# Optimization experiments

Measured on AMD Instinct MI355X. Metric: run time of the kernel, lower is better.

Reference implementation:

```python
import jax, jax.numpy as jnp
import numpy as np

N = 100000      # nodes
E = 1600000     # edges (avg degree 16)
IN = 128        # in_channels
HID = 64        # hidden_channels
OUT = 96


def setup_inputs() -> dict:
    key = jax.random.key(0)
    k = jax.random.split(key, 5)
    x = jax.random.normal(k[0], (N, IN), dtype=jnp.float32)
    edge_index = jax.random.randint(k[1], (2, E), 0, N, dtype=jnp.int64)
    # GCNConv weights (glorot-ish scale) and biases
    W1 = jax.random.normal(k[2], (IN, HID), dtype=jnp.float32) / np.sqrt(IN).astype(np.float32)
    b1 = jnp.zeros((HID,), dtype=jnp.float32)
    W2 = jax.random.normal(k[3], (HID, OUT), dtype=jnp.float32) / np.sqrt(HID).astype(np.float32)
    b2 = jnp.zeros((OUT,), dtype=jnp.float32)
    return {"x": x, "edge_index": edge_index, "W1": W1, "b1": b1, "W2": W2, "b2": b2}


def _gcn_conv(x, W, b, src, dst, norm):
    # linear transform, then degree-normalized gather-scale-scatter aggregation
    h = x @ W                                   # [N, F]
    msg = h[src] * norm[:, None]                # [E+N, F]
    agg = jax.ops.segment_sum(msg, dst, num_segments=N)  # [N, F]
    return agg + b


def reference(x, edge_index, W1, b1, W2, b2):
    # add self-loops (PyG GCNConv default add_self_loops=True)
    loops = jnp.arange(N, dtype=edge_index.dtype)
    src = jnp.concatenate([edge_index[0], loops])
    dst = jnp.concatenate([edge_index[1], loops])
    # symmetric normalization: deg computed over destination (col) with unit weights
    deg = jax.ops.segment_sum(jnp.ones_like(dst, dtype=x.dtype), dst, num_segments=N)
    dinv = jnp.where(deg > 0, jax.lax.rsqrt(deg), 0.0)
    norm = dinv[src] * dinv[dst]                # [E+N]
    h = jax.nn.relu(_gcn_conv(x, W1, b1, src, dst, norm))
    # dropout is identity in eval mode
    out = _gcn_conv(h, W2, b2, src, dst, norm)  # [N, OUT]
    return out
```

## Files before the change

### kernel.cpp

```cpp
#include <hip/hip_runtime.h>
#include <hip/hip_fp16.h>


#define IN_F  128
#define HID_F 64
#define OUT_F 96
#define CHUNK 4096
#define MAXB  12288
#define AGG_BLOCKS 4096
#define ONE_LO 0x00003C00u
#define ONE_HI 0x3C000000u

typedef _Float16 f16x2 __attribute__((ext_vector_type(2)));
typedef _Float16 half8 __attribute__((ext_vector_type(8)));
typedef float floatx4 __attribute__((ext_vector_type(4)));

__device__ __forceinline__ float2 unpack2(unsigned u) {
    __half2 h = *reinterpret_cast<__half2*>(&u);
    return __half22float2(h);
}
__device__ __forceinline__ unsigned f2h2(float lo, float hi) {
    __half2 h = __floats2half2_rn(lo, hi);
    return *reinterpret_cast<unsigned*>(&h);
}

#if defined(__has_builtin)
#if __has_builtin(__builtin_amdgcn_fdot2)
#define HAS_FDOT2 1
#endif
#if __has_builtin(__builtin_amdgcn_mfma_f32_16x16x32_f16)
#define HAS_MFMA 1
#endif
#endif
#ifndef HAS_FDOT2
#define HAS_FDOT2 0
#endif
#ifndef HAS_MFMA
#define HAS_MFMA 0
#endif

__device__ __forceinline__ float fdot2u(unsigned a, unsigned b, float c) {
#if HAS_FDOT2
    return __builtin_amdgcn_fdot2(__builtin_bit_cast(f16x2, a),
                                  __builtin_bit_cast(f16x2, b), c, false);
#else
    float2 fa = unpack2(a), fb = unpack2(b);
    return fmaf(fa.y, fb.y, fmaf(fa.x, fb.x, c));
#endif
}

__global__ __launch_bounds__(64) void init_sentinel(unsigned* __restrict__ hs,
                                                    unsigned* __restrict__ hs2, int n) {
    int t = threadIdx.x;
    if (t < 32) {
        hs[(size_t)n * 32 + t] = 0u;
        hs2[(size_t)n * 32 + t] = 0u;
    }
}

__global__ __launch_bounds__(256) void hist_chunks(const int* __restrict__ dst,
                                                   int* __restrict__ hist,
                                                   int E, int nbuck, int nchunk) {
    __shared__ int cnt[512];
    for (int i = threadIdx.x; i < nbuck; i += 256) cnt[i] = 0;
    __syncthreads();
    const int base = blockIdx.x * CHUNK;
    const int lim = min(base + CHUNK, E);
    for (int e = base + threadIdx.x; e < lim; e += 256)
        atomicAdd(&cnt[dst[e] >> 8], 1);
    __syncthreads();
    for (int b = threadIdx.x; b < nbuck; b += 256)
        hist[b * nchunk + blockIdx.x] = cnt[b];
}

__global__ __launch_bounds__(256) void scan_blocks(const int* __restrict__ in,
                                                   int* __restrict__ pre,
                                                   int* __restrict__ bsum, int m) {
    __shared__ int lds[256];
    const int t = threadIdx.x;
    const int base = blockIdx.x * 1024 + t * 4;
    int v0 = (base + 0 < m) ? in[base + 0] : 0;
    int v1 = (base + 1 < m) ? in[base + 1] : 0;
    int v2 = (base + 2 < m) ? in[base + 2] : 0;
    int v3 = (base + 3 < m) ? in[base + 3] : 0;
    int s = v0 + v1 + v2 + v3;
    lds[t] = s;
    __syncthreads();
    for (int off = 1; off < 256; off <<= 1) {
        int add = (t >= off) ? lds[t - off] : 0;
        __syncthreads();
        lds[t] += add;
        __syncthreads();
    }
    int e = lds[t] - s;
    if (base + 0 < m) pre[base + 0] = e;
    e += v0;
    if (base + 1 < m) pre[base + 1] = e;
    e += v1;
    if (base + 2 < m) pre[base + 2] = e;
    e += v2;
    if (base + 3 < m) pre[base + 3] = e;
    if (t == 255) bsum[blockIdx.x] = lds[255];
}

__global__ __launch_bounds__(256) void scan_bsums(const int* __restrict__ bsum,
                                                  int* __restrict__ boffs, int nb) {
    __shared__ int lds[256];
    const int t = threadIdx.x;
    int v = (t < nb) ? bsum[t] : 0;
    lds[t] = v;
    __syncthreads();
    for (int off = 1; off < 256; off <<= 1) {
        int add = (t >= off) ? lds[t - off] : 0;
        __syncthreads();
        lds[t] += add;
        __syncthreads();
    }
    boffs[t] = lds[t] - v;
}

__global__ __launch_bounds__(256) void partition(const int* __restrict__ src,
                                                 const int* __restrict__ dst,
                                                 const int* __restrict__ offs,
                                                 const int* __restrict__ boffs,
                                                 unsigned* __restrict__ part,
                                                 int E, int nbuck, int nchunk) {
    __shared__ int off[512];
    for (int b = threadIdx.x; b < nbuck; b += 256) {
        int idx = b * nchunk + blockIdx.x;
        off[b] = offs[idx] + boffs[idx >> 10];
    }
    __syncthreads();
    const int base = blockIdx.x * CHUNK;
    const int lim = min(base + CHUNK, E);
    for (int e = base + threadIdx.x; e < lim; e += 256) {
        int d = dst[e], s = src[e];
        int pos = atomicAdd(&off[d >> 8], 1);
        part[pos] = ((unsigned)s << 8) | (unsigned)(d & 255);
    }
}

__global__ __launch_bounds__(256) void build_bucket(const unsigned* __restrict__ part,
                                                    const int* __restrict__ offs,
                                                    const int* __restrict__ boffs,
                                                    int* __restrict__ csr_src,
                                                    int4* __restrict__ nodetab,
                                                    float* __restrict__ dinv,
                                                    int n, int E, int nbuck, int nchunk) {
    __shared__ int cnt[256], sc[256], off[256];
    __shared__ int stage[MAXB];
    const int b = blockIdx.x;
    const int t = threadIdx.x;
    const int i0 = b * nchunk;
    const int bstart = offs[i0] + boffs[i0 >> 10];
    int bend = E;
    if (b + 1 < nbuck) {
        const int i1 = (b + 1) * nchunk;
        bend = offs[i1] + boffs[i1 >> 10];
    }
    const int bstart_pad = bstart + b * 4096;
    const int nodebase = b << 8;
    const int nnodes = min(256, n - nodebase);

    cnt[t] = 0;
    __syncthreads();
    for (int i = bstart + t; i < bend; i += 256)
        atomicAdd(&cnt[part[i] & 255u], 1);
    __syncthreads();
    const int deg = cnt[t];
    const int pdeg = (deg + 15) & ~15;
    sc[t] = pdeg;
    __syncthreads();
    for (int o = 1; o < 256; o <<= 1) {
        int add = (t >= o) ? sc[t - o] : 0;
        __syncthreads();
        sc[t] += add;
        __syncthreads();
    }
    const int pexcl = sc[t] - pdeg;
    const int psize = sc[255];
    if (t < nnodes) {
        float dv = rsqrtf((float)(deg + 1));
        nodetab[nodebase + t] = make_int4(bstart_pad + pexcl,
                                          bstart_pad + pexcl + pdeg,
                                          __float_as_int(dv), 0);
        dinv[nodebase + t] = dv;
    }
    off[t] = pexcl;
    __syncthreads();

    if (psize <= MAXB) {
        for (int i = t; i < psize; i += 256) stage[i] = n;
        __syncthreads();
        for (int i = bstart + t; i < bend; i += 256) {
            unsigned r = part[i];
            int pos = atomicAdd(&off[r & 255u], 1);
            stage[pos] = (int)(r >> 8);
        }
        __syncthreads();
        for (int i = t; i < psize; i += 256)
            csr_src[bstart_pad + i] = stage[i];
    } else {
        for (int i = t; i < psize; i += 256) csr_src[bstart_pad + i] = n;
        __syncthreads();
        for (int i = bstart + t; i < bend; i += 256) {
            unsigned r = part[i];
            int pos = atomicAdd(&off[r & 255u], 1);
            csr_src[bstart_pad + pos] = (int)(r >> 8);
        }
    }
}

__global__ __launch_bounds__(256) void gemm1(const float* __restrict__ x,
                                             const float* __restrict__ W1,
                                             const float* __restrict__ dinv,
                                             unsigned* __restrict__ hs, int n) {
#if HAS_MFMA
    const int lane = threadIdx.x & 63;
    const int wave = threadIdx.x >> 6;
    const int q4 = lane >> 4;
    const int l16 = lane & 15;
    half8 bfrag[4][4];
#pragma unroll
    for (int ks = 0; ks < 4; ++ks)
#pragma unroll
        for (int cb = 0; cb < 4; ++cb)
#pragma unroll
            for (int j = 0; j < 8; ++j)
                bfrag[ks][cb][j] =
                    (_Float16)W1[(ks * 32 + q4 * 8 + j) * HID_F + cb * 16 + l16];

    const int ntile = (n + 15) >> 4;
    for (int t = blockIdx.x * 4 + wave; t < ntile; t += gridDim.x * 4) {
        const int r0 = t << 4;
        const int arow = min(r0 + l16, n - 1);
        const float* xr = x + (size_t)arow * IN_F + q4 * 8;
        half8 afrag[4];
#pragma unroll
        for (int ks = 0; ks < 4; ++ks) {
            float4 v0 = *(const float4*)(xr + ks * 32);
            float4 v1 = *(const float4*)(xr + ks * 32 + 4);
            half8 a;
            a[0] = (_Float16)v0.x; a[1] = (_Float16)v0.y;
            a[2] = (_Float16)v0.z; a[3] = (_Float16)v0.w;
            a[4] = (_Float16)v1.x; a[5] = (_Float16)v1.y;
            a[6] = (_Float16)v1.z; a[7] = (_Float16)v1.w;
            afrag[ks] = a;
        }
        floatx4 acc[4] = {{0.f,0.f,0.f,0.f},{0.f,0.f,0.f,0.f},
                          {0.f,0.f,0.f,0.f},{0.f,0.f,0.f,0.f}};
#pragma unroll
        for (int ks = 0; ks < 4; ++ks) {
#pragma unroll
            for (int cb = 0; cb < 4; ++cb)
                acc[cb] = __builtin_amdgcn_mfma_f32_16x16x32_f16(
                    afrag[ks], bfrag[ks][cb], acc[cb], 0, 0, 0);
        }
        const int rbase = r0 + q4 * 4;
        float4 dvv = *(const float4*)(dinv + rbase);
        float dvr[4] = {dvv.x, dvv.y, dvv.z, dvv.w};
#pragma unroll
        for (int cb = 0; cb < 4; ++cb) {
#pragma unroll
            for (int reg = 0; reg < 4; ++reg) {
                float v = acc[cb][reg] * dvr[reg];
                float o = __shfl_xor(v, 1);
                if (!(l16 & 1)) {
                    int r = rbase + reg;
                    if (r < n)
                        hs[(size_t)r * 32 + cb * 8 + (l16 >> 1)] = f2h2(v, o);
                }
            }
        }
    }
#endif
}

#define ACC2(u, slo, shi) { slo = fdot2u(u, ONE_LO, slo); shi = fdot2u(u, ONE_HI, shi); }
template <int LAYER>
__global__ __launch_bounds__(256) void csr_agg(const int4* __restrict__ nodetab,
                                               const int* __restrict__ csr_src,
                                               const unsigned* __restrict__ hs,
                                               const float* __restrict__ bias,
                                               unsigned* __restrict__ hout, int n) {
    const int lane = threadIdx.x & 63;
    const int g = lane >> 4;
    const int w = lane & 15;
    const unsigned* __restrict__ hw = hs + 2 * w;
    const int STR = gridDim.x * 16;
    const int SENT = n;

    for (int base = (blockIdx.x * 4 + (threadIdx.x >> 6)) * 4; base < n; base += STR) {
        int pp0, pp1, pp2, pp3, ee0, ee1, ee2, ee3;
        float dn0, dn1, dn2, dn3;
        {
            int4 nt0 = nodetab[base];
            pp0 = nt0.x; ee0 = nt0.y; dn0 = __int_as_float(nt0.z);
        }
        if (base + 1 < n) { int4 v = nodetab[base + 1]; pp1 = v.x; ee1 = v.y; dn1 = __int_as_float(v.z); }
        else { pp1 = 0; ee1 = 0; dn1 = 0.f; }
        if (base + 2 < n) { int4 v = nodetab[base + 2]; pp2 = v.x; ee2 = v.y; dn2 = __int_as_float(v.z); }
        else { pp2 = 0; ee2 = 0; dn2 = 0.f; }
        if (base + 3 < n) { int4 v = nodetab[base + 3]; pp3 = v.x; ee3 = v.y; dn3 = __int_as_float(v.z); }
        else { pp3 = 0; ee3 = 0; dn3 = 0.f; }

        float a00 = 0.f, a01 = 0.f, a02 = 0.f, a03 = 0.f;
        float a10 = 0.f, a11 = 0.f, a12 = 0.f, a13 = 0.f;
        float a20 = 0.f, a21 = 0.f, a22 = 0.f, a23 = 0.f;
        float a30 = 0.f, a31 = 0.f, a32 = 0.f, a33 = 0.f;
        if (g == 0) {
            int s0 = base;
            int s1 = (base + 1 < n) ? base + 1 : SENT;
            int s2 = (base + 2 < n) ? base + 2 : SENT;
            int s3 = (base + 3 < n) ? base + 3 : SENT;
            uint2 u0 = *(const uint2*)(hw + (size_t)s0 * 32);
            uint2 u1 = *(const uint2*)(hw + (size_t)s1 * 32);
            uint2 u2 = *(const uint2*)(hw + (size_t)s2 * 32);
            uint2 u3 = *(const uint2*)(hw + (size_t)s3 * 32);
            ACC2(u0.x, a00, a01); ACC2(u0.y, a02, a03);
            ACC2(u1.x, a10, a11); ACC2(u1.y, a12, a13);
            ACC2(u2.x, a20, a21); ACC2(u2.y, a22, a23);
            ACC2(u3.x, a30, a31); ACC2(u3.y, a32, a33);
        }
        while ((pp0 < ee0) | (pp1 < ee1) | (pp2 < ee2) | (pp3 < ee3)) {
            int4 iv0 = (pp0 < ee0) ? *(const int4*)&csr_src[pp0 + 4 * g]
                                   : make_int4(SENT, SENT, SENT, SENT);
            int4 iv1 = (pp1 < ee1) ? *(const int4*)&csr_src[pp1 + 4 * g]
                                   : make_int4(SENT, SENT, SENT, SENT);
            int4 iv2 = (pp2 < ee2) ? *(const int4*)&csr_src[pp2 + 4 * g]
                                   : make_int4(SENT, SENT, SENT, SENT);
            int4 iv3 = (pp3 < ee3) ? *(const int4*)&csr_src[pp3 + 4 * g]
                                   : make_int4(SENT, SENT, SENT, SENT);
            uint2 u00 = *(const uint2*)(hw + (size_t)iv0.x * 32);
            uint2 u01 = *(const uint2*)(hw + (size_t)iv0.y * 32);
            uint2 u02 = *(const uint2*)(hw + (size_t)iv0.z * 32);
            uint2 u03 = *(const uint2*)(hw + (size_t)iv0.w * 32);
            uint2 u10 = *(const uint2*)(hw + (size_t)iv1.x * 32);
            uint2 u11 = *(const uint2*)(hw + (size_t)iv1.y * 32);
            uint2 u12 = *(const uint2*)(hw + (size_t)iv1.z * 32);
            uint2 u13 = *(const uint2*)(hw + (size_t)iv1.w * 32);
            uint2 u20 = *(const uint2*)(hw + (size_t)iv2.x * 32);
            uint2 u21 = *(const uint2*)(hw + (size_t)iv2.y * 32);
            uint2 u22 = *(const uint2*)(hw + (size_t)iv2.z * 32);
            uint2 u23 = *(const uint2*)(hw + (size_t)iv2.w * 32);
            uint2 u30 = *(const uint2*)(hw + (size_t)iv3.x * 32);
            uint2 u31 = *(const uint2*)(hw + (size_t)iv3.y * 32);
            uint2 u32 = *(const uint2*)(hw + (size_t)iv3.z * 32);
            uint2 u33 = *(const uint2*)(hw + (size_t)iv3.w * 32);
            ACC2(u00.x, a00, a01); ACC2(u00.y, a02, a03);
            ACC2(u01.x, a00, a01); ACC2(u01.y, a02, a03);
            ACC2(u02.x, a00, a01); ACC2(u02.y, a02, a03);
            ACC2(u03.x, a00, a01); ACC2(u03.y, a02, a03);
            ACC2(u10.x, a10, a11); ACC2(u10.y, a12, a13);
            ACC2(u11.x, a10, a11); ACC2(u11.y, a12, a13);
            ACC2(u12.x, a10, a11); ACC2(u12.y, a12, a13);
            ACC2(u13.x, a10, a11); ACC2(u13.y, a12, a13);
            ACC2(u20.x, a20, a21); ACC2(u20.y, a22, a23);
            ACC2(u21.x, a20, a21); ACC2(u21.y, a22, a23);
            ACC2(u22.x, a20, a21); ACC2(u22.y, a22, a23);
            ACC2(u23.x, a20, a21); ACC2(u23.y, a22, a23);
            ACC2(u30.x, a30, a31); ACC2(u30.y, a32, a33);
            ACC2(u31.x, a30, a31); ACC2(u31.y, a32, a33);
            ACC2(u32.x, a30, a31); ACC2(u32.y, a32, a33);
            ACC2(u33.x, a30, a31); ACC2(u33.y, a32, a33);
            pp0 += 16; pp1 += 16; pp2 += 16; pp3 += 16;
        }
        a00 += __shfl_xor(a00, 16); a00 += __shfl_xor(a00, 32);
        a01 += __shfl_xor(a01, 16); a01 += __shfl_xor(a01, 32);
        a02 += __shfl_xor(a02, 16); a02 += __shfl_xor(a02, 32);
        a03 += __shfl_xor(a03, 16); a03 += __shfl_xor(a03, 32);
        a10 += __shfl_xor(a10, 16); a10 += __shfl_xor(a10, 32);
        a11 += __shfl_xor(a11, 16); a11 += __shfl_xor(a11, 32);
        a12 += __shfl_xor(a12, 16); a12 += __shfl_xor(a12, 32);
        a13 += __shfl_xor(a13, 16); a13 += __shfl_xor(a13, 32);
        a20 += __shfl_xor(a20, 16); a20 += __shfl_xor(a20, 32);
        a21 += __shfl_xor(a21, 16); a21 += __shfl_xor(a21, 32);
        a22 += __shfl_xor(a22, 16); a22 += __shfl_xor(a22, 32);
        a23 += __shfl_xor(a23, 16); a23 += __shfl_xor(a23, 32);
        a30 += __shfl_xor(a30, 16); a30 += __shfl_xor(a30, 32);
        a31 += __shfl_xor(a31, 16); a31 += __shfl_xor(a31, 32);
        a32 += __shfl_xor(a32, 16); a32 += __shfl_xor(a32, 32);
        a33 += __shfl_xor(a33, 16); a33 += __shfl_xor(a33, 32);

        if (g == 0) {
            float4 bb;
            if (LAYER == 1) bb = *(const float4*)(bias + 4 * w);
#define EPI(i, dn, v0, v1, v2, v3)                                          \
            if (base + i < n) {                                             \
                float o0, o1, o2, o3;                                       \
                if (LAYER == 1) {                                           \
                    o0 = fmaxf(fmaf(dn, v0, bb.x), 0.f) * dn;               \
                    o1 = fmaxf(fmaf(dn, v1, bb.y), 0.f) * dn;               \
                    o2 = fmaxf(fmaf(dn, v2, bb.z), 0.f) * dn;               \
                    o3 = fmaxf(fmaf(dn, v3, bb.w), 0.f) * dn;               \
                } else {                                                    \
                    o0 = dn * v0; o1 = dn * v1; o2 = dn * v2; o3 = dn * v3; \
                }                                                           \
                uint2 ov;                                                   \
                ov.x = f2h2(o0, o1);                                        \
                ov.y = f2h2(o2, o3);                                        \
                *(uint2*)(hout + (size_t)(base + i) * 32 + 2 * w) = ov;     \
            }
            EPI(0, dn0, a00, a01, a02, a03)
            EPI(1, dn1, a10, a11, a12, a13)
            EPI(2, dn2, a20, a21, a22, a23)
            EPI(3, dn3, a30, a31, a32, a33)
#undef EPI
        }
    }
}

__global__ __launch_bounds__(256) void gemm2(const unsigned* __restrict__ a2h,
                                             const float* __restrict__ W2,
                                             const float* __restrict__ b2,
                                             float* __restrict__ out, int n) {
#if HAS_MFMA
    const int lane = threadIdx.x & 63;
    const int wave = threadIdx.x >> 6;
    const int q4 = lane >> 4;
    const int l16 = lane & 15;
    half8 bfrag[2][6];
#pragma unroll
    for (int ks = 0; ks < 2; ++ks)
#pragma unroll
        for (int cb = 0; cb < 6; ++cb)
#pragma unroll
            for (int j = 0; j < 8; ++j)
                bfrag[ks][cb][j] =
                    (_Float16)W2[(ks * 32 + q4 * 8 + j) * OUT_F + cb * 16 + l16];
    float bb[6];
#pragma unroll
    for (int cb = 0; cb < 6; ++cb) bb[cb] = b2[cb * 16 + l16];

    const int ntile = (n + 15) >> 4;
    for (int t = blockIdx.x * 4 + wave; t < ntile; t += gridDim.x * 4) {
        const int r0 = t << 4;
        const int arow = min(r0 + l16, n - 1);
        const unsigned* ar = a2h + (size_t)arow * 32;
        half8 afrag[2];
#pragma unroll
        for (int ks = 0; ks < 2; ++ks) {
            uint4 v = *(const uint4*)(ar + ks * 16 + q4 * 4);
            afrag[ks] = __builtin_bit_cast(half8, v);
        }
        floatx4 acc[6] = {{0.f,0.f,0.f,0.f},{0.f,0.f,0.f,0.f},{0.f,0.f,0.f,0.f},
                          {0.f,0.f,0.f,0.f},{0.f,0.f,0.f,0.f},{0.f,0.f,0.f,0.f}};
#pragma unroll
        for (int ks = 0; ks < 2; ++ks) {
#pragma unroll
            for (int cb = 0; cb < 6; ++cb)
                acc[cb] = __builtin_amdgcn_mfma_f32_16x16x32_f16(
                    afrag[ks], bfrag[ks][cb], acc[cb], 0, 0, 0);
        }
        const int rbase = r0 + q4 * 4;
#pragma unroll
        for (int reg = 0; reg < 4; ++reg) {
            int r = rbase + reg;
            if (r < n) {
#pragma unroll
                for (int cb = 0; cb < 6; ++cb)
                    out[(size_t)r * OUT_F + cb * 16 + l16] = acc[cb][reg] + bb[cb];
            }
        }
    }
#endif
}

extern "C" void kernel_launch(void* const* d_in, const int* in_sizes, int n_in,
                              void* d_out, int out_size, void* d_ws, size_t ws_size,
                              hipStream_t stream) {
    const float* x  = (const float*)d_in[0];
    const int*   ei = (const int*)d_in[1];
    const float* W1 = (const float*)d_in[2];
    const float* b1 = (const float*)d_in[3];
    const float* W2 = (const float*)d_in[4];
    const float* b2 = (const float*)d_in[5];
    float* out = (float*)d_out;

    const int n = in_sizes[0] / IN_F;
    const int E = in_sizes[1] / 2;
    const int* src = ei;
    const int* dst = ei + E;
    const int nbuck  = (n + 255) >> 8;
    const int nchunk = (E + CHUNK - 1) / CHUNK;
    const int M = nbuck * nchunk;
    const int NBS = (M + 1023) / 1024;
    const int g1tiles = (n + 15) / 16;
    const int g1blocks = (g1tiles + 7) / 8;

    char* ws = (char*)d_ws;
    size_t off = 0;
    auto alloc = [&](size_t bytes) { void* p = ws + off; off = (off + bytes + 255) & ~(size_t)255; return p; };
    int*      hist    = (int*)alloc((size_t)M * 4);
    int*      offs    = (int*)alloc((size_t)M * 4);
    int*      bsum    = (int*)alloc(256 * 4);
    int*      boffs   = (int*)alloc(256 * 4);
    unsigned* part    = (unsigned*)alloc((size_t)E * 4);
    int*      csr_src = (int*)alloc(((size_t)E + (size_t)nbuck * 4096 + 64) * 4);
    int4*     nodetab = (int4*)alloc((size_t)n * 16);
    float*    dinv    = (float*)alloc((size_t)n * 4);
    unsigned* hs      = (unsigned*)alloc((size_t)(n + 1) * 32 * 4);
    unsigned* hs2     = (unsigned*)alloc((size_t)(n + 1) * 32 * 4);
    unsigned* a2h     = (unsigned*)alloc((size_t)n * 32 * 4);

    init_sentinel<<<1, 64, 0, stream>>>(hs, hs2, n);
    hist_chunks <<<nchunk, 256, 0, stream>>>(dst, hist, E, nbuck, nchunk);
    scan_blocks <<<NBS, 256, 0, stream>>>(hist, offs, bsum, M);
    scan_bsums  <<<1, 256, 0, stream>>>(bsum, boffs, NBS);
    partition   <<<nchunk, 256, 0, stream>>>(src, dst, offs, boffs, part, E, nbuck, nchunk);
    build_bucket<<<nbuck, 256, 0, stream>>>(part, offs, boffs, csr_src, nodetab, dinv,
                                            n, E, nbuck, nchunk);

    gemm1      <<<g1blocks, 256, 0, stream>>>(x, W1, dinv, hs, n);
    csr_agg<1> <<<AGG_BLOCKS, 256, 0, stream>>>(nodetab, csr_src, hs, b1, hs2, n);
    csr_agg<2> <<<AGG_BLOCKS, 256, 0, stream>>>(nodetab, csr_src, hs2, NULL, a2h, n);
    gemm2      <<<g1blocks, 256, 0, stream>>>(a2h, W2, b2, out, n);
}
```

Before: 158.9 us.

## Restructure CSR aggregation to 2 nodes per wave with 16-byte row gathers

The aggregation kernel now gives each wave 2 nodes instead of 4. Each row is split over 8 lanes that each load a uint4 (16 B) instead of 16 lanes loading uint2, so each lane group consumes 2 edges per step and 8 groups cover 16 edges. It also prefetches the next node-table entries before processing the current pair, to hide that latency. The aim is wider gather loads, fewer wasted sentinel loads on imbalanced degrees, and overlapped index fetching. In exchange the shuffle reduction gains a stage, there is less memory-level parallelism per wave, and a grid-stride loop with software prefetch is added.

```diff
diff --git a/kernel.cpp b/kernel.cpp
--- a/kernel.cpp
+++ b/kernel.cpp
@@ -284,129 +284,134 @@
                                                const float* __restrict__ bias,
                                                unsigned* __restrict__ hout, int n) {
     const int lane = threadIdx.x & 63;
-    const int g = lane >> 4;
-    const int w = lane & 15;
-    const unsigned* __restrict__ hw = hs + 2 * w;
-    const int STR = gridDim.x * 16;
+    const int g = lane >> 3;
+    const int w = lane & 7;
+    const uint4* __restrict__ hw4 = (const uint4*)hs + w;
+    const int STR = gridDim.x * 8;
     const int SENT = n;
 
-    for (int base = (blockIdx.x * 4 + (threadIdx.x >> 6)) * 4; base < n; base += STR) {
-        int pp0, pp1, pp2, pp3, ee0, ee1, ee2, ee3;
-        float dn0, dn1, dn2, dn3;
-        {
-            int4 nt0 = nodetab[base];
-            pp0 = nt0.x; ee0 = nt0.y; dn0 = __int_as_float(nt0.z);
-        }
-        if (base + 1 < n) { int4 v = nodetab[base + 1]; pp1 = v.x; ee1 = v.y; dn1 = __int_as_float(v.z); }
-        else { pp1 = 0; ee1 = 0; dn1 = 0.f; }
-        if (base + 2 < n) { int4 v = nodetab[base + 2]; pp2 = v.x; ee2 = v.y; dn2 = __int_as_float(v.z); }
-        else { pp2 = 0; ee2 = 0; dn2 = 0.f; }
-        if (base + 3 < n) { int4 v = nodetab[base + 3]; pp3 = v.x; ee3 = v.y; dn3 = __int_as_float(v.z); }
-        else { pp3 = 0; ee3 = 0; dn3 = 0.f; }
-
-        float a00 = 0.f, a01 = 0.f, a02 = 0.f, a03 = 0.f;
-        float a10 = 0.f, a11 = 0.f, a12 = 0.f, a13 = 0.f;
-        float a20 = 0.f, a21 = 0.f, a22 = 0.f, a23 = 0.f;
-        float a30 = 0.f, a31 = 0.f, a32 = 0.f, a33 = 0.f;
+    int nodeA = (blockIdx.x * 4 + (threadIdx.x >> 6)) * 2;
+    if (nodeA >= n) return;
+    int4 ntA = nodetab[nodeA];
+    bool hasB = nodeA + 1 < n;
+    int4 ntB = hasB ? nodetab[nodeA + 1] : make_int4(0, 0, 0, 0);
+
+    for (;;) {
+        const int nxt = nodeA + STR;
+        const bool more = nxt < n;
+        int4 ntA_n, ntB_n;
+        bool hasB_n = false;
+        if (more) {
+            ntA_n = nodetab[nxt];
+            hasB_n = nxt + 1 < n;
+            if (hasB_n) ntB_n = nodetab[nxt + 1];
+        }
+
+        int pA = ntA.x;
+        const int endA = ntA.y;
+        const float dnA = __int_as_float(ntA.z);
+        int pB = hasB ? ntB.x : 0;
+        const int endB = hasB ? ntB.y : 0;
+        const float dnB = hasB ? __int_as_float(ntB.z) : 0.f;
+
+        float aA0 = 0.f, aA1 = 0.f, aA2 = 0.f, aA3 = 0.f;
+        float aA4 = 0.f, aA5 = 0.f, aA6 = 0.f, aA7 = 0.f;
+        float aB0 = 0.f, aB1 = 0.f, aB2 = 0.f, aB3 = 0.f;
+        float aB4 = 0.f, aB5 = 0.f, aB6 = 0.f, aB7 = 0.f;
         if (g == 0) {
-            int s0 = base;
-            int s1 = (base + 1 < n) ? base + 1 : SENT;
-            int s2 = (base + 2 < n) ? base + 2 : SENT;
-            int s3 = (base + 3 < n) ? base + 3 : SENT;
-            uint2 u0 = *(const uint2*)(hw + (size_t)s0 * 32);
-            uint2 u1 = *(const uint2*)(hw + (size_t)s1 * 32);
-            uint2 u2 = *(const uint2*)(hw + (size_t)s2 * 32);
-            uint2 u3 = *(const uint2*)(hw + (size_t)s3 * 32);
-            ACC2(u0.x, a00, a01); ACC2(u0.y, a02, a03);
-            ACC2(u1.x, a10, a11); ACC2(u1.y, a12, a13);
-            ACC2(u2.x, a20, a21); ACC2(u2.y, a22, a23);
-            ACC2(u3.x, a30, a31); ACC2(u3.y, a32, a33);
-        }
-        while ((pp0 < ee0) | (pp1 < ee1) | (pp2 < ee2) | (pp3 < ee3)) {
-            int4 iv0 = (pp0 < ee0) ? *(const int4*)&csr_src[pp0 + 4 * g]
-                                   : make_int4(SENT, SENT, SENT, SENT);
-            int4 iv1 = (pp1 < ee1) ? *(const int4*)&csr_src[pp1 + 4 * g]
-                                   : make_int4(SENT, SENT, SENT, SENT);
-            int4 iv2 = (pp2 < ee2) ? *(const int4*)&csr_src[pp2 + 4 * g]
-                                   : make_int4(SENT, SENT, SENT, SENT);
-            int4 iv3 = (pp3 < ee3) ? *(const int4*)&csr_src[pp3 + 4 * g]
-                                   : make_int4(SENT, SENT, SENT, SENT);
-            uint2 u00 = *(const uint2*)(hw + (size_t)iv0.x * 32);
-            uint2 u01 = *(const uint2*)(hw + (size_t)iv0.y * 32);
-            uint2 u02 = *(const uint2*)(hw + (size_t)iv0.z * 32);
-            uint2 u03 = *(const uint2*)(hw + (size_t)iv0.w * 32);
-            uint2 u10 = *(const uint2*)(hw + (size_t)iv1.x * 32);
-            uint2 u11 = *(const uint2*)(hw + (size_t)iv1.y * 32);
-            uint2 u12 = *(const uint2*)(hw + (size_t)iv1.z * 32);
-            uint2 u13 = *(const uint2*)(hw + (size_t)iv1.w * 32);
-            uint2 u20 = *(const uint2*)(hw + (size_t)iv2.x * 32);
-            uint2 u21 = *(const uint2*)(hw + (size_t)iv2.y * 32);
-            uint2 u22 = *(const uint2*)(hw + (size_t)iv2.z * 32);
-            uint2 u23 = *(const uint2*)(hw + (size_t)iv2.w * 32);
-            uint2 u30 = *(const uint2*)(hw + (size_t)iv3.x * 32);
-            uint2 u31 = *(const uint2*)(hw + (size_t)iv3.y * 32);
-            uint2 u32 = *(const uint2*)(hw + (size_t)iv3.z * 32);
-            uint2 u33 = *(const uint2*)(hw + (size_t)iv3.w * 32);
-            ACC2(u00.x, a00, a01); ACC2(u00.y, a02, a03);
-            ACC2(u01.x, a00, a01); ACC2(u01.y, a02, a03);
-            ACC2(u02.x, a00, a01); ACC2(u02.y, a02, a03);
-            ACC2(u03.x, a00, a01); ACC2(u03.y, a02, a03);
-            ACC2(u10.x, a10, a11); ACC2(u10.y, a12, a13);
-            ACC2(u11.x, a10, a11); ACC2(u11.y, a12, a13);
-            ACC2(u12.x, a10, a11); ACC2(u12.y, a12, a13);
-            ACC2(u13.x, a10, a11); ACC2(u13.y, a12, a13);
-            ACC2(u20.x, a20, a21); ACC2(u20.y, a22, a23);
-            ACC2(u21.x, a20, a21); ACC2(u21.y, a22, a23);
-            ACC2(u22.x, a20, a21); ACC2(u22.y, a22, a23);
-            ACC2(u23.x, a20, a21); ACC2(u23.y, a22, a23);
-            ACC2(u30.x, a30, a31); ACC2(u30.y, a32, a33);
-            ACC2(u31.x, a30, a31); ACC2(u31.y, a32, a33);
-            ACC2(u32.x, a30, a31); ACC2(u32.y, a32, a33);
-            ACC2(u33.x, a30, a31); ACC2(u33.y, a32, a33);
-            pp0 += 16; pp1 += 16; pp2 += 16; pp3 += 16;
-        }
-        a00 += __shfl_xor(a00, 16); a00 += __shfl_xor(a00, 32);
-        a01 += __shfl_xor(a01, 16); a01 += __shfl_xor(a01, 32);
-        a02 += __shfl_xor(a02, 16); a02 += __shfl_xor(a02, 32);
-        a03 += __shfl_xor(a03, 16); a03 += __shfl_xor(a03, 32);
-        a10 += __shfl_xor(a10, 16); a10 += __shfl_xor(a10, 32);
-        a11 += __shfl_xor(a11, 16); a11 += __shfl_xor(a11, 32);
-        a12 += __shfl_xor(a12, 16); a12 += __shfl_xor(a12, 32);
-        a13 += __shfl_xor(a13, 16); a13 += __shfl_xor(a13, 32);
-        a20 += __shfl_xor(a20, 16); a20 += __shfl_xor(a20, 32);
-        a21 += __shfl_xor(a21, 16); a21 += __shfl_xor(a21, 32);
-        a22 += __shfl_xor(a22, 16); a22 += __shfl_xor(a22, 32);
-        a23 += __shfl_xor(a23, 16); a23 += __shfl_xor(a23, 32);
-        a30 += __shfl_xor(a30, 16); a30 += __shfl_xor(a30, 32);
-        a31 += __shfl_xor(a31, 16); a31 += __shfl_xor(a31, 32);
-        a32 += __shfl_xor(a32, 16); a32 += __shfl_xor(a32, 32);
-        a33 += __shfl_xor(a33, 16); a33 += __shfl_xor(a33, 32);
+            uint4 suA = hw4[(size_t)nodeA * 8];
+            ACC2(suA.x, aA0, aA1); ACC2(suA.y, aA2, aA3);
+            ACC2(suA.z, aA4, aA5); ACC2(suA.w, aA6, aA7);
+            if (hasB) {
+                uint4 suB = hw4[(size_t)(nodeA + 1) * 8];
+                ACC2(suB.x, aB0, aB1); ACC2(suB.y, aB2, aB3);
+                ACC2(suB.z, aB4, aB5); ACC2(suB.w, aB6, aB7);
+            }
+        }
+        while (pA < endA || pB < endB) {
+            int2 ivA = (pA < endA) ? *(const int2*)&csr_src[pA + 2 * g]
+                                   : make_int2(SENT, SENT);
+            int2 ivB = (pB < endB) ? *(const int2*)&csr_src[pB + 2 * g]
+                                   : make_int2(SENT, SENT);
+            uint4 uA0 = hw4[(size_t)ivA.x * 8];
+            uint4 uA1 = hw4[(size_t)ivA.y * 8];
+            uint4 uB0 = hw4[(size_t)ivB.x * 8];
+            uint4 uB1 = hw4[(size_t)ivB.y * 8];
+            ACC2(uA0.x, aA0, aA1); ACC2(uA0.y, aA2, aA3);
+            ACC2(uA0.z, aA4, aA5); ACC2(uA0.w, aA6, aA7);
+            ACC2(uA1.x, aA0, aA1); ACC2(uA1.y, aA2, aA3);
+            ACC2(uA1.z, aA4, aA5); ACC2(uA1.w, aA6, aA7);
+            ACC2(uB0.x, aB0, aB1); ACC2(uB0.y, aB2, aB3);
+            ACC2(uB0.z, aB4, aB5); ACC2(uB0.w, aB6, aB7);
+            ACC2(uB1.x, aB0, aB1); ACC2(uB1.y, aB2, aB3);
+            ACC2(uB1.z, aB4, aB5); ACC2(uB1.w, aB6, aB7);
+            pA += 16; pB += 16;
+        }
+        aA0 += __shfl_xor(aA0, 8); aA0 += __shfl_xor(aA0, 16); aA0 += __shfl_xor(aA0, 32);
+        aA1 += __shfl_xor(aA1, 8); aA1 += __shfl_xor(aA1, 16); aA1 += __shfl_xor(aA1, 32);
+        aA2 += __shfl_xor(aA2, 8); aA2 += __shfl_xor(aA2, 16); aA2 += __shfl_xor(aA2, 32);
+        aA3 += __shfl_xor(aA3, 8); aA3 += __shfl_xor(aA3, 16); aA3 += __shfl_xor(aA3, 32);
+        aA4 += __shfl_xor(aA4, 8); aA4 += __shfl_xor(aA4, 16); aA4 += __shfl_xor(aA4, 32);
+        aA5 += __shfl_xor(aA5, 8); aA5 += __shfl_xor(aA5, 16); aA5 += __shfl_xor(aA5, 32);
+        aA6 += __shfl_xor(aA6, 8); aA6 += __shfl_xor(aA6, 16); aA6 += __shfl_xor(aA6, 32);
+        aA7 += __shfl_xor(aA7, 8); aA7 += __shfl_xor(aA7, 16); aA7 += __shfl_xor(aA7, 32);
+        aB0 += __shfl_xor(aB0, 8); aB0 += __shfl_xor(aB0, 16); aB0 += __shfl_xor(aB0, 32);
+        aB1 += __shfl_xor(aB1, 8); aB1 += __shfl_xor(aB1, 16); aB1 += __shfl_xor(aB1, 32);
+        aB2 += __shfl_xor(aB2, 8); aB2 += __shfl_xor(aB2, 16); aB2 += __shfl_xor(aB2, 32);
+        aB3 += __shfl_xor(aB3, 8); aB3 += __shfl_xor(aB3, 16); aB3 += __shfl_xor(aB3, 32);
+        aB4 += __shfl_xor(aB4, 8); aB4 += __shfl_xor(aB4, 16); aB4 += __shfl_xor(aB4, 32);
+        aB5 += __shfl_xor(aB5, 8); aB5 += __shfl_xor(aB5, 16); aB5 += __shfl_xor(aB5, 32);
+        aB6 += __shfl_xor(aB6, 8); aB6 += __shfl_xor(aB6, 16); aB6 += __shfl_xor(aB6, 32);
+        aB7 += __shfl_xor(aB7, 8); aB7 += __shfl_xor(aB7, 16); aB7 += __shfl_xor(aB7, 32);
 
         if (g == 0) {
-            float4 bb;
-            if (LAYER == 1) bb = *(const float4*)(bias + 4 * w);
-#define EPI(i, dn, v0, v1, v2, v3)                                          \
-            if (base + i < n) {                                             \
-                float o0, o1, o2, o3;                                       \
-                if (LAYER == 1) {                                           \
-                    o0 = fmaxf(fmaf(dn, v0, bb.x), 0.f) * dn;               \
-                    o1 = fmaxf(fmaf(dn, v1, bb.y), 0.f) * dn;               \
-                    o2 = fmaxf(fmaf(dn, v2, bb.z), 0.f) * dn;               \
-                    o3 = fmaxf(fmaf(dn, v3, bb.w), 0.f) * dn;               \
-                } else {                                                    \
-                    o0 = dn * v0; o1 = dn * v1; o2 = dn * v2; o3 = dn * v3; \
-                }                                                           \
-                uint2 ov;                                                   \
-                ov.x = f2h2(o0, o1);                                        \
-                ov.y = f2h2(o2, o3);                                        \
-                *(uint2*)(hout + (size_t)(base + i) * 32 + 2 * w) = ov;     \
+            float4 bb0, bb1;
+            if (LAYER == 1) {
+                bb0 = *(const float4*)(bias + 8 * w);
+                bb1 = *(const float4*)(bias + 8 * w + 4);
             }
-            EPI(0, dn0, a00, a01, a02, a03)
-            EPI(1, dn1, a10, a11, a12, a13)
-            EPI(2, dn2, a20, a21, a22, a23)
-            EPI(3, dn3, a30, a31, a32, a33)
-#undef EPI
-        }
+            float o0, o1, o2, o3, o4, o5, o6, o7;
+            if (LAYER == 1) {
+                o0 = fmaxf(fmaf(dnA, aA0, bb0.x), 0.f) * dnA;
+                o1 = fmaxf(fmaf(dnA, aA1, bb0.y), 0.f) * dnA;
+                o2 = fmaxf(fmaf(dnA, aA2, bb0.z), 0.f) * dnA;
+                o3 = fmaxf(fmaf(dnA, aA3, bb0.w), 0.f) * dnA;
+                o4 = fmaxf(fmaf(dnA, aA4, bb1.x), 0.f) * dnA;
+                o5 = fmaxf(fmaf(dnA, aA5, bb1.y), 0.f) * dnA;
+                o6 = fmaxf(fmaf(dnA, aA6, bb1.z), 0.f) * dnA;
+                o7 = fmaxf(fmaf(dnA, aA7, bb1.w), 0.f) * dnA;
+            } else {
+                o0 = dnA * aA0; o1 = dnA * aA1; o2 = dnA * aA2; o3 = dnA * aA3;
+                o4 = dnA * aA4; o5 = dnA * aA5; o6 = dnA * aA6; o7 = dnA * aA7;
+            }
+            uint4 ov;
+            ov.x = f2h2(o0, o1); ov.y = f2h2(o2, o3);
+            ov.z = f2h2(o4, o5); ov.w = f2h2(o6, o7);
+            *(uint4*)(hout + (size_t)nodeA * 32 + 4 * w) = ov;
+            if (hasB) {
+                if (LAYER == 1) {
+                    o0 = fmaxf(fmaf(dnB, aB0, bb0.x), 0.f) * dnB;
+                    o1 = fmaxf(fmaf(dnB, aB1, bb0.y), 0.f) * dnB;
+                    o2 = fmaxf(fmaf(dnB, aB2, bb0.z), 0.f) * dnB;
+                    o3 = fmaxf(fmaf(dnB, aB3, bb0.w), 0.f) * dnB;
+                    o4 = fmaxf(fmaf(dnB, aB4, bb1.x), 0.f) * dnB;
+                    o5 = fmaxf(fmaf(dnB, aB5, bb1.y), 0.f) * dnB;
+                    o6 = fmaxf(fmaf(dnB, aB6, bb1.z), 0.f) * dnB;
+                    o7 = fmaxf(fmaf(dnB, aB7, bb1.w), 0.f) * dnB;
+                } else {
+                    o0 = dnB * aB0; o1 = dnB * aB1; o2 = dnB * aB2; o3 = dnB * aB3;
+                    o4 = dnB * aB4; o5 = dnB * aB5; o6 = dnB * aB6; o7 = dnB * aB7;
+                }
+                ov.x = f2h2(o0, o1); ov.y = f2h2(o2, o3);
+                ov.z = f2h2(o4, o5); ov.w = f2h2(o6, o7);
+                *(uint4*)(hout + (size_t)(nodeA + 1) * 32 + 4 * w) = ov;
+            }
+        }
+        if (!more) break;
+        nodeA = nxt;
+        ntA = ntA_n;
+        hasB = hasB_n;
+        ntB = ntB_n;
     }
 }
 
```

Result: faster. 151.7 us (-4.5%).
